# Kernel optimization log

Measured on AMD Instinct MI355X. Metric: run time of the kernel, lower is better.

Reference implementation:

```python
import jax, jax.numpy as jnp
import numpy as np

EMBED_DIM = 1024
NUM_HEADS = 16
HEAD_DIM = EMBED_DIM // NUM_HEADS
FF_DIM = 4096
EPS = 1e-5


def layer_norm(x, gamma, beta):
    mu = jnp.mean(x, axis=-1, keepdims=True)
    var = jnp.var(x, axis=-1, keepdims=True)
    return (x - mu) * jax.lax.rsqrt(var + EPS) * gamma + beta


def setup_inputs() -> dict:
    key = jax.random.key(0)
    ks = jax.random.split(key, 10)
    B, S = 2, 2048
    sd = 1.0 / np.sqrt(EMBED_DIM)
    sf = 1.0 / np.sqrt(FF_DIM)
    return {
        "x": jax.random.normal(ks[0], (B, S, EMBED_DIM), jnp.float32),
        # grouped QKV: 3*num_heads groups, each embed_dim -> head_dim
        "Wqkv": jax.random.normal(ks[1], (3 * NUM_HEADS, EMBED_DIM, HEAD_DIM), jnp.float32) * sd,
        "bqkv": jnp.zeros((3 * NUM_HEADS, HEAD_DIM), jnp.float32),
        "Wo": jax.random.normal(ks[2], (EMBED_DIM, EMBED_DIM), jnp.float32) * sd,
        "bo": jnp.zeros((EMBED_DIM,), jnp.float32),
        "W1": jax.random.normal(ks[3], (EMBED_DIM, FF_DIM), jnp.float32) * sd,
        "b1": jnp.zeros((FF_DIM,), jnp.float32),
        "W2": jax.random.normal(ks[4], (FF_DIM, EMBED_DIM), jnp.float32) * sf,
        "b2": jnp.zeros((EMBED_DIM,), jnp.float32),
        "ln1_g": jnp.ones((EMBED_DIM,), jnp.float32),
        "ln1_b": jnp.zeros((EMBED_DIM,), jnp.float32),
        "ln2_g": jnp.ones((EMBED_DIM,), jnp.float32),
        "ln2_b": jnp.zeros((EMBED_DIM,), jnp.float32),
    }


def reference(x, Wqkv, bqkv, Wo, bo, W1, b1, W2, b2, ln1_g, ln1_b, ln2_g, ln2_b):
    B, S, D = x.shape
    normed = layer_norm(x, ln1_g, ln1_b)
    # grouped QKV projection: group g gets its own (D, head_dim) weight
    qkv = jnp.einsum('bsd,gdh->bgsh', normed, Wqkv) + bqkv[None, :, None, :]
    qkv = qkv.reshape(B, 3, NUM_HEADS, S, HEAD_DIM)
    q, k, v = qkv[:, 0], qkv[:, 1], qkv[:, 2]  # each [B, H, S, hd]
    attn = jnp.einsum('bhqd,bhkd->bhqk', q, k) / np.sqrt(HEAD_DIM)
    attn = jax.nn.softmax(attn, axis=-1)
    out = jnp.einsum('bhqk,bhkd->bhqd', attn, v)
    out = out.transpose(0, 2, 1, 3).reshape(B, S, D)
    out = out @ Wo + bo
    x = x + out
    normed2 = layer_norm(x, ln2_g, ln2_b)
    ff = jax.nn.relu(normed2 @ W1 + b1) @ W2 + b2
    return x + ff
```

## Files before the change

### kernel.cpp

```cpp
#include <hip/hip_runtime.h>
#include <stdint.h>

#define SEQ    2048
#define NB     2
#define NHEADS 16
#define HDIM   64
#define EMBED  1024
#define NROWS  (NB*SEQ)
#define QKVSZ  ((size_t)NB*NHEADS*SEQ*HDIM)

typedef __attribute__((ext_vector_type(8))) short short8;
typedef __attribute__((ext_vector_type(4))) float float4v;
typedef __attribute__((ext_vector_type(16))) float float16v;
typedef __attribute__((ext_vector_type(2))) unsigned int uint2v;
typedef __attribute__((ext_vector_type(4))) unsigned int uint4v;

__device__ __forceinline__ float b2f(unsigned short h) {
    unsigned int u = ((unsigned int)h) << 16;
    union { unsigned int u; float f; } c; c.u = u; return c.f;
}
__device__ __forceinline__ unsigned short f2b(float f) {
    union { float f; unsigned int u; } c; c.f = f;
    unsigned int u = c.u;
    u += 0x7FFFu + ((u >> 16) & 1u);
    return (unsigned short)(u >> 16);
}
__device__ __forceinline__ unsigned int fbits(float f) {
    union { float f; unsigned int u; } c; c.f = f; return c.u;
}
__device__ __forceinline__ unsigned int cvtpk_bf16(float lo, float hi) {
    unsigned int r;
    asm("v_cvt_pk_bf16_f32 %0, %1, %2" : "=v"(r) : "v"(lo), "v"(hi));
    return r;
}

__device__ __forceinline__ void gload_lds16(const void* g, void* l) {
    __builtin_amdgcn_global_load_lds(
        (const __attribute__((address_space(1))) unsigned int*)g,
        (__attribute__((address_space(3))) unsigned int*)l, 16, 0, 0);
}

__device__ __forceinline__ int probe_f32(const void* probe) {
    return ((const unsigned short*)probe)[0] == 0;
}
__device__ __forceinline__ float lde(const void* base, size_t off, int f32) {
    return f32 ? ((const float*)base)[off] : b2f(((const unsigned short*)base)[off]);
}
__device__ __forceinline__ void ste(void* base, size_t off, float v, int f32) {
    if (f32) ((float*)base)[off] = v;
    else     ((unsigned short*)base)[off] = f2b(v);
}

__global__ __launch_bounds__(256) void ln_kernel(
    const void* __restrict__ x,
    const void* __restrict__ g,
    const void* __restrict__ b,
    unsigned short* __restrict__ out,
    const void* __restrict__ probe)
{
    int f32 = probe_f32(probe);
    int row = blockIdx.x;
    int t = threadIdx.x;
    float v0, v1, v2, v3;
    if (f32) {
        float4 rv = ((const float4*)x)[(size_t)row * (EMBED / 4) + t];
        v0 = rv.x; v1 = rv.y; v2 = rv.z; v3 = rv.w;
    } else {
        ushort4 rv = ((const ushort4*)((const unsigned short*)x + (size_t)row * EMBED))[t];
        v0 = b2f(rv.x); v1 = b2f(rv.y); v2 = b2f(rv.z); v3 = b2f(rv.w);
    }
    float s  = v0 + v1 + v2 + v3;
    float sq = v0*v0 + v1*v1 + v2*v2 + v3*v3;
    #pragma unroll
    for (int off = 32; off > 0; off >>= 1) {
        s  += __shfl_xor(s,  off);
        sq += __shfl_xor(sq, off);
    }
    __shared__ float red[8];
    int lane = t & 63, wv = t >> 6;
    if (lane == 0) { red[wv] = s; red[wv + 4] = sq; }
    __syncthreads();
    s  = red[0] + red[1] + red[2] + red[3];
    sq = red[4] + red[5] + red[6] + red[7];
    float mu  = s * (1.0f / EMBED);
    float var = sq * (1.0f / EMBED) - mu * mu;
    float rs  = rsqrtf(var + 1e-5f);
    float g0 = lde(g, t*4+0, f32), g1 = lde(g, t*4+1, f32);
    float g2 = lde(g, t*4+2, f32), g3 = lde(g, t*4+3, f32);
    float b0 = lde(b, t*4+0, f32), b1 = lde(b, t*4+1, f32);
    float b2 = lde(b, t*4+2, f32), b3 = lde(b, t*4+3, f32);
    ushort4 ov;
    ov.x = f2b((v0 - mu) * rs * g0 + b0);
    ov.y = f2b((v1 - mu) * rs * g1 + b1);
    ov.z = f2b((v2 - mu) * rs * g2 + b2);
    ov.w = f2b((v3 - mu) * rs * g3 + b3);
    ((ushort4*)(out + (size_t)row * EMBED))[t] = ov;
}

template<int QKV>
__global__ __launch_bounds__(256) void transpose_kernel(
    const void* __restrict__ in,
    unsigned short* __restrict__ out, int K, int N,
    const void* __restrict__ probe)
{
    __shared__ unsigned short t[64 * 68];
    int f32 = probe_f32(probe);
    int tid = threadIdx.x;
    int n0 = blockIdx.x * 64, k0 = blockIdx.y * 64;
    #pragma unroll
    for (int i = 0; i < 4; i++) {
        int id = tid + i * 256;
        int kr = id >> 4, nc = (id & 15) * 4;
        size_t srcoff;
        if (QKV) srcoff = ((size_t)(n0 >> 6) << 16) + (size_t)(k0 + kr) * 64 + nc;
        else     srcoff = (size_t)(k0 + kr) * N + n0 + nc;
        ushort4 val;
        if (f32) {
            float4 rv = *(const float4*)((const float*)in + srcoff);
            val.x = f2b(rv.x); val.y = f2b(rv.y); val.z = f2b(rv.z); val.w = f2b(rv.w);
        } else {
            val = *(const ushort4*)((const unsigned short*)in + srcoff);
        }
        *(ushort4*)&t[kr * 68 + nc] = val;
    }
    __syncthreads();
    #pragma unroll
    for (int i = 0; i < 4; i++) {
        int id = tid + i * 256;
        int nr = id >> 4, kc = (id & 15) * 4;
        ushort4 o;
        o.x = t[(kc + 0) * 68 + nr];
        o.y = t[(kc + 1) * 68 + nr];
        o.z = t[(kc + 2) * 68 + nr];
        o.w = t[(kc + 3) * 68 + nr];
        *(ushort4*)(out + (size_t)(n0 + nr) * K + k0 + kc) = o;
    }
}

template<int DO_RELU, int HAS_BIAS, int OUTMODE>
__global__ __launch_bounds__(512) void gemm256_kernel(
    const unsigned short* __restrict__ A,
    const unsigned short* __restrict__ Bt,
    const void* __restrict__ bias,
    void* __restrict__ out,
    int M, int N, int Kloc, int ldA, int ldB,
    const void* __restrict__ probe)
{
    __shared__ unsigned short Als[2][256 * 64];
    __shared__ unsigned short Bls[2][256 * 64];
    int f32 = probe_f32(probe);
    int tid = threadIdx.x;
    int lane = tid & 63, wv = tid >> 6;
    int lq = lane >> 4, lr = lane & 15;
    int wr = wv >> 2, wc = wv & 3;
    int m0 = blockIdx.y * 256, n0 = blockIdx.x * 256;
    int k0 = blockIdx.z * Kloc;

    int srow = tid >> 3;
    int sch  = (tid & 7) ^ (srow & 7);
    const unsigned short* ga = A  + (size_t)(m0 + srow) * ldA + k0 + sch * 8;
    const unsigned short* gb = Bt + (size_t)(n0 + srow) * ldB + k0 + sch * 8;
    int ldst = tid * 8;
    int rx = lr & 7;

    float4v acc[8][4];
    #pragma unroll
    for (int i = 0; i < 8; i++)
        #pragma unroll
        for (int j = 0; j < 4; j++)
            { acc[i][j][0] = 0.f; acc[i][j][1] = 0.f; acc[i][j][2] = 0.f; acc[i][j][3] = 0.f; }

    int nkt = Kloc >> 6;
    #pragma unroll
    for (int u = 0; u < 4; u++)
        gload_lds16(ga + (size_t)u * 64 * ldA, &Als[0][u * 4096 + ldst]);
    #pragma unroll
    for (int u = 0; u < 4; u++)
        gload_lds16(gb + (size_t)u * 64 * ldB, &Bls[0][u * 4096 + ldst]);

    for (int kt = 0; kt < nkt; kt++) {
        int cur = kt & 1, nxt = cur ^ 1;
        if (kt + 1 < nkt) {
            int ko = (kt + 1) * 64;
            #pragma unroll
            for (int u = 0; u < 4; u++)
                gload_lds16(ga + (size_t)u * 64 * ldA + ko, &Als[nxt][u * 4096 + ldst]);
            asm volatile("s_waitcnt vmcnt(4)" ::: "memory");
        } else {
            asm volatile("s_waitcnt vmcnt(0)" ::: "memory");
        }
        __builtin_amdgcn_s_barrier();
        asm volatile("" ::: "memory");
        {
            short8 af[8], bf[4];
            #pragma unroll
            for (int mt = 0; mt < 8; mt++)
                af[mt] = *(const short8*)(
                    &Als[cur][(wr * 128 + mt * 16 + lr) * 64 + ((lq ^ rx) * 8)]);
            #pragma unroll
            for (int nt = 0; nt < 4; nt++)
                bf[nt] = *(const short8*)(
                    &Bls[cur][(wc * 64 + nt * 16 + lr) * 64 + ((lq ^ rx) * 8)]);
            __builtin_amdgcn_s_setprio(1);
            #pragma unroll
            for (int mt = 0; mt < 8; mt++)
                #pragma unroll
                for (int nt = 0; nt < 4; nt++)
                    acc[mt][nt] = __builtin_amdgcn_mfma_f32_16x16x32_bf16(af[mt], bf[nt], acc[mt][nt], 0, 0, 0);
            __builtin_amdgcn_s_setprio(0);
        }
        if (kt + 1 < nkt) {
            int ko = (kt + 1) * 64;
            #pragma unroll
            for (int u = 0; u < 4; u++)
                gload_lds16(gb + (size_t)u * 64 * ldB + ko, &Bls[nxt][u * 4096 + ldst]);
        }
        {
            short8 af[8], bf[4];
            #pragma unroll
            for (int mt = 0; mt < 8; mt++)
                af[mt] = *(const short8*)(
                    &Als[cur][(wr * 128 + mt * 16 + lr) * 64 + (((4 + lq) ^ rx) * 8)]);
            #pragma unroll
            for (int nt = 0; nt < 4; nt++)
                bf[nt] = *(const short8*)(
                    &Bls[cur][(wc * 64 + nt * 16 + lr) * 64 + (((4 + lq) ^ rx) * 8)]);
            __builtin_amdgcn_s_setprio(1);
            #pragma unroll
            for (int mt = 0; mt < 8; mt++)
                #pragma unroll
                for (int nt = 0; nt < 4; nt++)
                    acc[mt][nt] = __builtin_amdgcn_mfma_f32_16x16x32_bf16(af[mt], bf[nt], acc[mt][nt], 0, 0, 0);
            __builtin_amdgcn_s_setprio(0);
        }
        asm volatile("s_waitcnt lgkmcnt(0)" ::: "memory");
        __builtin_amdgcn_s_barrier();
    }

    if (OUTMODE == 3) {
        float* po = (float*)out + (size_t)blockIdx.z * M * N;
        #pragma unroll
        for (int mt = 0; mt < 8; mt++)
            #pragma unroll
            for (int nt = 0; nt < 4; nt++)
                #pragma unroll
                for (int rg = 0; rg < 4; rg++) {
                    int rr = m0 + wr * 128 + mt * 16 + lq * 4 + rg;
                    int cc = n0 + wc * 64 + nt * 16 + lr;
                    po[(size_t)rr * N + cc] = acc[mt][nt][rg];
                }
    } else if (OUTMODE == 2) {
        #pragma unroll
        for (int mt = 0; mt < 8; mt++) {
            int rrb = m0 + wr * 128 + mt * 16 + lq * 4;
            int bb = rrb >> 11, ss = rrb & 2047;
            #pragma unroll
            for (int nt = 0; nt < 4; nt++) {
                int cc = n0 + wc * 64 + nt * 16 + lr;
                int gg = cc >> 6, hd = cc & 63;
                int ty = gg >> 4, hh = gg & 15;
                float vv[4];
                #pragma unroll
                for (int rg = 0; rg < 4; rg++) {
                    float v = acc[mt][nt][rg];
                    if (HAS_BIAS) v += lde(bias, (size_t)cc, f32);
                    vv[rg] = v;
                }
                if (ty < 2) {
                    unsigned short* p = (unsigned short*)out + (size_t)ty * QKVSZ +
                        (((size_t)(bb * NHEADS + hh) * SEQ + ss) * HDIM) + hd;
                    #pragma unroll
                    for (int rg = 0; rg < 4; rg++) p[(size_t)rg * HDIM] = f2b(vv[rg]);
                } else {
                    ushort4 pk;
                    pk.x = f2b(vv[0]); pk.y = f2b(vv[1]);
                    pk.z = f2b(vv[2]); pk.w = f2b(vv[3]);
                    *(ushort4*)((unsigned short*)out + 2 * QKVSZ +
                        ((size_t)(bb * NHEADS + hh) * HDIM + hd) * SEQ + ss) = pk;
                }
            }
        }
    } else {
        #pragma unroll
        for (int mt = 0; mt < 8; mt++)
            #pragma unroll
            for (int nt = 0; nt < 4; nt++)
                #pragma unroll
                for (int rg = 0; rg < 4; rg++) {
                    int rr = m0 + wr * 128 + mt * 16 + lq * 4 + rg;
                    int cc = n0 + wc * 64 + nt * 16 + lr;
                    float v = acc[mt][nt][rg];
                    if (HAS_BIAS) v += lde(bias, (size_t)cc, f32);
                    if (DO_RELU) v = v > 0.f ? v : 0.f;
                    ((unsigned short*)out)[(size_t)rr * N + cc] = f2b(v);
                }
    }
}

__global__ __launch_bounds__(256) void ff2_combine_kernel(
    const float* __restrict__ part,
    const void* __restrict__ b2,
    void* __restrict__ xout,
    const void* __restrict__ probe)
{
    int f32 = probe_f32(probe);
    int row = blockIdx.x;
    int t = threadIdx.x;
    const size_t MN = (size_t)NROWS * EMBED;
    size_t base = (size_t)row * EMBED + t * 4;
    float4 p0 = *(const float4*)(part + base);
    float4 p1 = *(const float4*)(part + MN + base);
    float4 p2 = *(const float4*)(part + 2 * MN + base);
    float4 p3 = *(const float4*)(part + 3 * MN + base);
    float s0 = (p0.x + p1.x) + (p2.x + p3.x);
    float s1 = (p0.y + p1.y) + (p2.y + p3.y);
    float s2 = (p0.z + p1.z) + (p2.z + p3.z);
    float s3 = (p0.w + p1.w) + (p2.w + p3.w);
    int c = t * 4;
    s0 += lde(b2, c + 0, f32) + lde(xout, base + 0, f32);
    s1 += lde(b2, c + 1, f32) + lde(xout, base + 1, f32);
    s2 += lde(b2, c + 2, f32) + lde(xout, base + 2, f32);
    s3 += lde(b2, c + 3, f32) + lde(xout, base + 3, f32);
    ste(xout, base + 0, s0, f32);
    ste(xout, base + 1, s1, f32);
    ste(xout, base + 2, s2, f32);
    ste(xout, base + 3, s3, f32);
}

template<int DO_RELU, int HAS_BIAS, int HAS_RES, int OUTMODE>
__global__ __launch_bounds__(256) void gemm64_kernel(
    const unsigned short* __restrict__ A,
    const unsigned short* __restrict__ Bt,
    const void* __restrict__ bias,
    const void* __restrict__ res,
    void* __restrict__ out,
    int M, int N, int K, int ldA, int ldB,
    const void* __restrict__ probe)
{
    __shared__ unsigned short Als[2][64 * 32];
    __shared__ unsigned short Bls[2][64 * 32];
    int f32 = probe_f32(probe);
    int tid = threadIdx.x;
    int lane = tid & 63, wv = tid >> 6;
    int lq = lane >> 4, lr = lane & 15;
    int moff = (wv >> 1) * 32, noff = (wv & 1) * 32;
    int m0 = blockIdx.y * 64, n0 = blockIdx.x * 64;

    int rA = tid >> 2, jA = tid & 3;
    int jjA = jA ^ ((rA >> 1) & 3);
    const unsigned short* ga = A  + (size_t)(m0 + rA) * ldA + jjA * 8;
    const unsigned short* gb = Bt + (size_t)(n0 + rA) * ldB + jjA * 8;

    int fch = (lq ^ ((lr >> 1) & 3)) * 8;

    float4v acc[2][2];
    #pragma unroll
    for (int i = 0; i < 2; i++)
        #pragma unroll
        for (int j = 0; j < 2; j++)
            { acc[i][j][0] = 0.f; acc[i][j][1] = 0.f; acc[i][j][2] = 0.f; acc[i][j][3] = 0.f; }

    gload_lds16(ga, &Als[0][(size_t)tid * 8]);
    gload_lds16(gb, &Bls[0][(size_t)tid * 8]);

    int nkt = K >> 5;
    for (int kt = 0; kt < nkt; kt++) {
        int cur = kt & 1, nxt = cur ^ 1;
        __syncthreads();
        if (kt + 1 < nkt) {
            int ko = (kt + 1) * 32;
            gload_lds16(ga + ko, &Als[nxt][(size_t)tid * 8]);
            gload_lds16(gb + ko, &Bls[nxt][(size_t)tid * 8]);
        }
        short8 af[2], bfr[2];
        #pragma unroll
        for (int mt = 0; mt < 2; mt++)
            af[mt] = *(const short8*)(&Als[cur][(moff + mt * 16 + lr) * 32 + fch]);
        #pragma unroll
        for (int nt = 0; nt < 2; nt++)
            bfr[nt] = *(const short8*)(&Bls[cur][(noff + nt * 16 + lr) * 32 + fch]);
        #pragma unroll
        for (int mt = 0; mt < 2; mt++)
            #pragma unroll
            for (int nt = 0; nt < 2; nt++)
                acc[mt][nt] = __builtin_amdgcn_mfma_f32_16x16x32_bf16(af[mt], bfr[nt], acc[mt][nt], 0, 0, 0);
    }

    #pragma unroll
    for (int mt = 0; mt < 2; mt++) {
        #pragma unroll
        for (int nt = 0; nt < 2; nt++) {
            #pragma unroll
            for (int rg = 0; rg < 4; rg++) {
                int rr = m0 + moff + mt * 16 + lq * 4 + rg;
                int cc = n0 + noff + nt * 16 + lr;
                float v = acc[mt][nt][rg];
                if (HAS_BIAS) v += lde(bias, (size_t)cc, f32);
                if (DO_RELU) v = v > 0.f ? v : 0.f;
                if (HAS_RES) v += lde(res, (size_t)rr * N + cc, f32);
                if (OUTMODE == 1) ste(out, (size_t)rr * N + cc, v, f32);
                else ((unsigned short*)out)[(size_t)rr * N + cc] = f2b(v);
            }
        }
    }
}

__global__ __launch_bounds__(256) void attn_kernel(
    const unsigned short* __restrict__ qb,
    const unsigned short* __restrict__ kb,
    const unsigned short* __restrict__ vtb,
    unsigned short* __restrict__ outb)
{
    __shared__ unsigned short Kls[2][64 * 64];
    __shared__ unsigned short Vls[2][64 * 64];
    int tid = threadIdx.x;
    int lane = tid & 63, wv = tid >> 6;
    int l31 = lane & 31, hh = lane >> 5;
    int bh = blockIdx.y;
    int b = bh >> 4, head = bh & 15;
    const unsigned short* q  = qb  + (size_t)bh * SEQ * HDIM;
    const unsigned short* k  = kb  + (size_t)bh * SEQ * HDIM;
    const unsigned short* vt = vtb + (size_t)bh * HDIM * SEQ;
    int q0w = blockIdx.x * 128 + wv * 32;

    const float C2 = 0.18033688011112042f;

    short8 qf[4];
    #pragma unroll
    for (int c = 0; c < 4; c++) {
        short8 raw = *(const short8*)(q + (size_t)(q0w + l31) * HDIM + c * 16 + hh * 8);
        #pragma unroll
        for (int j = 0; j < 8; j++)
            qf[c][j] = (short)f2b(b2f((unsigned short)raw[j]) * C2);
    }

    int rS = tid >> 3;
    int jjS = (tid & 7) ^ (rS & 7);
    const unsigned short* gk0 = k + (size_t)rS * HDIM + jjS * 8;
    const unsigned short* gk1 = k + (size_t)(rS + 32) * HDIM + jjS * 8;
    const unsigned short* gv0 = vt + (size_t)rS * SEQ + jjS * 8;
    const unsigned short* gv1 = vt + (size_t)(rS + 32) * SEQ + jjS * 8;

    float l_part = 0.f;
    float16v o0, o1;
    #pragma unroll
    for (int i = 0; i < 16; i++) { o0[i] = 0.f; o1[i] = 0.f; }

    gload_lds16(gk0, &Kls[0][(size_t)tid * 8]);
    gload_lds16(gk1, &Kls[0][(size_t)(tid + 256) * 8]);
    gload_lds16(gv0, &Vls[0][(size_t)tid * 8]);
    gload_lds16(gv1, &Vls[0][(size_t)(tid + 256) * 8]);

    for (int kt = 0; kt < SEQ / 64; kt++) {
        int cur = kt & 1, nxt = cur ^ 1;
        __syncthreads();
        if (kt + 1 < SEQ / 64) {
            int k0n = (kt + 1) * 64;
            gload_lds16(gk0 + (size_t)k0n * HDIM, &Kls[nxt][(size_t)tid * 8]);
            gload_lds16(gk1 + (size_t)k0n * HDIM, &Kls[nxt][(size_t)(tid + 256) * 8]);
            gload_lds16(gv0 + k0n, &Vls[nxt][(size_t)tid * 8]);
            gload_lds16(gv1 + k0n, &Vls[nxt][(size_t)(tid + 256) * 8]);
        }

        #pragma unroll
        for (int kb2 = 0; kb2 < 2; kb2++) {
            float16v st;
            #pragma unroll
            for (int i = 0; i < 16; i++) st[i] = 0.f;
            int r = kb2 * 32 + l31;
            int rx = r & 7;
            #pragma unroll
            for (int c = 0; c < 4; c++) {
                short8 kf = *(const short8*)(
                    &Kls[cur][r * 64 + (((2 * c + hh) ^ rx) * 8)]);
                st = __builtin_amdgcn_mfma_f32_32x32x16_bf16(kf, qf[c], st, 0, 0, 0);
            }
            float p[16];
            #pragma unroll
            for (int rg = 0; rg < 16; rg++) {
                p[rg] = __builtin_amdgcn_exp2f(st[rg]);
                l_part += p[rg];
            }
            int rv0 = l31, rv1 = 32 + l31;
            int rxv = l31 & 7;
            #pragma unroll
            for (int s = 0; s < 2; s++) {
                unsigned int a1 = cvtpk_bf16(p[8*s+0], p[8*s+1]);
                unsigned int a2 = cvtpk_bf16(p[8*s+2], p[8*s+3]);
                unsigned int b1 = cvtpk_bf16(p[8*s+4], p[8*s+5]);
                unsigned int b2 = cvtpk_bf16(p[8*s+6], p[8*s+7]);
                uint2v r1 = __builtin_amdgcn_permlane32_swap(a1, b1, false, false);
                uint2v r2 = __builtin_amdgcn_permlane32_swap(a2, b2, false, false);
                union { uint4v u; short8 s8; } pun;
                pun.u.x = r1.x; pun.u.y = r2.x; pun.u.z = r1.y; pun.u.w = r2.y;
                short8 pf = pun.s8;
                int g = kb2 * 2 + s;
                short8 vf0 = *(const short8*)(
                    &Vls[cur][rv0 * 64 + (((2 * g + hh) ^ rxv) * 8)]);
                o0 = __builtin_amdgcn_mfma_f32_32x32x16_bf16(pf, vf0, o0, 0, 0, 0);
                short8 vf1 = *(const short8*)(
                    &Vls[cur][rv1 * 64 + (((2 * g + hh) ^ rxv) * 8)]);
                o1 = __builtin_amdgcn_mfma_f32_32x32x16_bf16(pf, vf1, o1, 0, 0, 0);
            }
        }
    }

    l_part += __shfl_xor(l_part, 32);
    float linv_me = 1.f / l_part;
    #pragma unroll
    for (int rg = 0; rg < 16; rg++) {
        int qrow = (rg & 3) + 8 * (rg >> 2) + 4 * hh;
        float linv = __shfl(linv_me, qrow);
        size_t rowbase = ((size_t)(b * SEQ + q0w + qrow)) * EMBED + head * HDIM;
        outb[rowbase + l31]      = f2b(o0[rg] * linv);
        outb[rowbase + 32 + l31] = f2b(o1[rg] * linv);
    }
}

extern "C" void kernel_launch(void* const* d_in, const int* in_sizes, int n_in,
                              void* d_out, int out_size, void* d_ws, size_t ws_size,
                              hipStream_t stream)
{
    (void)in_sizes; (void)n_in; (void)out_size;
    const void* x    = d_in[0];
    const void* Wqkv = d_in[1];
    const void* bqkv = d_in[2];
    const void* Wo   = d_in[3];
    const void* bo   = d_in[4];
    const void* W1   = d_in[5];
    const void* b1   = d_in[6];
    const void* W2   = d_in[7];
    const void* b2   = d_in[8];
    const void* g1   = d_in[9];
    const void* be1  = d_in[10];
    const void* g2   = d_in[11];
    const void* be2  = d_in[12];
    const void* probe = g1;

    char* ws = (char*)d_ws;
    const size_t MB = 1024 * 1024;
    unsigned short* tmp1  = (unsigned short*)(ws + 0 * MB);
    unsigned short* qkv   = (unsigned short*)(ws + 8 * MB);
    unsigned short* WoT   = (unsigned short*)(ws + 8 * MB);
    unsigned short* W1T   = (unsigned short*)(ws + 8 * MB);
    unsigned short* W2T   = (unsigned short*)(ws + 8 * MB);
    unsigned short* h1    = (unsigned short*)(ws + 16 * MB);
    float*          part  = (float*)(ws + 48 * MB);
    unsigned short* WqkvT = (unsigned short*)d_out;
    bool splitk_ok = ws_size >= (size_t)112 * MB;

    transpose_kernel<1><<<dim3(3072 / 64, 1024 / 64), 256, 0, stream>>>(Wqkv, WqkvT, 1024, 3072, probe);
    ln_kernel<<<dim3(NROWS), 256, 0, stream>>>(x, g1, be1, tmp1, probe);
    gemm256_kernel<0, 1, 2><<<dim3(3072 / 256, NROWS / 256), 512, 0, stream>>>(
        tmp1, WqkvT, bqkv, qkv, NROWS, 3072, 1024, 1024, 1024, probe);
    attn_kernel<<<dim3(SEQ / 128, NB * NHEADS), 256, 0, stream>>>(
        qkv, qkv + QKVSZ, qkv + 2 * QKVSZ, tmp1);
    transpose_kernel<0><<<dim3(1024 / 64, 1024 / 64), 256, 0, stream>>>(Wo, WoT, 1024, 1024, probe);
    gemm64_kernel<0, 1, 1, 1><<<dim3(1024 / 64, NROWS / 64), 256, 0, stream>>>(
        tmp1, WoT, bo, x, d_out, NROWS, 1024, 1024, 1024, 1024, probe);
    ln_kernel<<<dim3(NROWS), 256, 0, stream>>>(d_out, g2, be2, tmp1, probe);
    transpose_kernel<0><<<dim3(4096 / 64, 1024 / 64), 256, 0, stream>>>(W1, W1T, 1024, 4096, probe);
    gemm256_kernel<1, 1, 0><<<dim3(4096 / 256, NROWS / 256), 512, 0, stream>>>(
        tmp1, W1T, b1, h1, NROWS, 4096, 1024, 1024, 1024, probe);
    transpose_kernel<0><<<dim3(1024 / 64, 4096 / 64), 256, 0, stream>>>(W2, W2T, 4096, 1024, probe);
    if (splitk_ok) {
        gemm256_kernel<0, 0, 3><<<dim3(1024 / 256, NROWS / 256, 4), 512, 0, stream>>>(
            h1, W2T, nullptr, part, NROWS, 1024, 1024, 4096, 4096, probe);
        ff2_combine_kernel<<<dim3(NROWS), 256, 0, stream>>>(part, b2, d_out, probe);
    } else {
        gemm64_kernel<0, 1, 1, 1><<<dim3(1024 / 64, NROWS / 64), 256, 0, stream>>>(
            h1, W2T, b2, d_out, d_out, NROWS, 1024, 4096, 4096, 4096, probe);
    }
}
```

Baseline: 390.4 us.

## Split 256x256 GEMM tile into four 128x128 quadrant phases with staged prefetch

Restructures the 256x256 bf16 GEMM main loop into four quadrant phases, each computing a 128x128 sub-tile of the output. A and B are loaded into LDS as 128-row halves, and the prefetch of the next K-tile is interleaved across the phases with finer-grained vmcnt waits and barriers. The goal is to overlap global-to-LDS loads with MFMA work more evenly and to reuse A/B fragments held in registers across adjacent quadrants. The cost is four times as many barriers per K-step and a more fragile schedule that depends on wait counts.

```diff
diff --git a/kernel.cpp b/kernel.cpp
--- a/kernel.cpp
+++ b/kernel.cpp
@@ -146,8 +146,8 @@
     int M, int N, int Kloc, int ldA, int ldB,
     const void* __restrict__ probe)
 {
-    __shared__ unsigned short Als[2][256 * 64];
-    __shared__ unsigned short Bls[2][256 * 64];
+    __shared__ unsigned short Als[2][2][128 * 64];
+    __shared__ unsigned short Bls[2][2][128 * 64];
     int f32 = probe_f32(probe);
     int tid = threadIdx.x;
     int lane = tid & 63, wv = tid >> 6;
@@ -163,138 +163,166 @@
     int ldst = tid * 8;
     int rx = lr & 7;
 
-    float4v acc[8][4];
-    #pragma unroll
-    for (int i = 0; i < 8; i++)
-        #pragma unroll
-        for (int j = 0; j < 4; j++)
-            { acc[i][j][0] = 0.f; acc[i][j][1] = 0.f; acc[i][j][2] = 0.f; acc[i][j][3] = 0.f; }
+    auto stageA = [&](int d, int h, int ko) {
+        gload_lds16(ga + (size_t)(h * 128) * ldA + ko, &Als[d][h][ldst]);
+        gload_lds16(ga + (size_t)(h * 128 + 64) * ldA + ko, &Als[d][h][4096 + ldst]);
+    };
+    auto stageB = [&](int d, int h, int ko) {
+        gload_lds16(gb + (size_t)(h * 128) * ldB + ko, &Bls[d][h][ldst]);
+        gload_lds16(gb + (size_t)(h * 128 + 64) * ldB + ko, &Bls[d][h][4096 + ldst]);
+    };
+    auto rdA = [&](int cur_, int qr, short8 (&af)[4][2]) {
+        #pragma unroll
+        for (int mt = 0; mt < 4; mt++)
+            #pragma unroll
+            for (int c = 0; c < 2; c++)
+                af[mt][c] = *(const short8*)(&Als[cur_][qr][
+                    (wr * 64 + mt * 16 + lr) * 64 + (((c * 4 + lq) ^ rx) * 8)]);
+    };
+    auto rdB = [&](int cur_, int qc, short8 (&bf)[2][2]) {
+        #pragma unroll
+        for (int nt = 0; nt < 2; nt++)
+            #pragma unroll
+            for (int c = 0; c < 2; c++)
+                bf[nt][c] = *(const short8*)(&Bls[cur_][qc][
+                    (wc * 32 + nt * 16 + lr) * 64 + (((c * 4 + lq) ^ rx) * 8)]);
+    };
+    auto FMA = [&](short8 (&af)[4][2], short8 (&bf)[2][2], float4v (&aq)[4][2]) {
+        __builtin_amdgcn_s_setprio(1);
+        #pragma unroll
+        for (int c = 0; c < 2; c++)
+            #pragma unroll
+            for (int mt = 0; mt < 4; mt++)
+                #pragma unroll
+                for (int nt = 0; nt < 2; nt++)
+                    aq[mt][nt] = __builtin_amdgcn_mfma_f32_16x16x32_bf16(
+                        af[mt][c], bf[nt][c], aq[mt][nt], 0, 0, 0);
+        __builtin_amdgcn_s_setprio(0);
+    };
+
+    float4v acc00[4][2], acc01[4][2], acc11[4][2], acc10[4][2];
+    #pragma unroll
+    for (int i = 0; i < 4; i++)
+        #pragma unroll
+        for (int j = 0; j < 2; j++) {
+            acc00[i][j] = float4v{0.f, 0.f, 0.f, 0.f};
+            acc01[i][j] = float4v{0.f, 0.f, 0.f, 0.f};
+            acc11[i][j] = float4v{0.f, 0.f, 0.f, 0.f};
+            acc10[i][j] = float4v{0.f, 0.f, 0.f, 0.f};
+        }
 
     int nkt = Kloc >> 6;
-    #pragma unroll
-    for (int u = 0; u < 4; u++)
-        gload_lds16(ga + (size_t)u * 64 * ldA, &Als[0][u * 4096 + ldst]);
-    #pragma unroll
-    for (int u = 0; u < 4; u++)
-        gload_lds16(gb + (size_t)u * 64 * ldB, &Bls[0][u * 4096 + ldst]);
+    stageA(0, 0, 0); stageB(0, 0, 0); stageB(0, 1, 0); stageA(0, 1, 0);
 
     for (int kt = 0; kt < nkt; kt++) {
         int cur = kt & 1, nxt = cur ^ 1;
-        if (kt + 1 < nkt) {
-            int ko = (kt + 1) * 64;
-            #pragma unroll
-            for (int u = 0; u < 4; u++)
-                gload_lds16(ga + (size_t)u * 64 * ldA + ko, &Als[nxt][u * 4096 + ldst]);
-            asm volatile("s_waitcnt vmcnt(4)" ::: "memory");
-        } else {
-            asm volatile("s_waitcnt vmcnt(0)" ::: "memory");
-        }
-        __builtin_amdgcn_s_barrier();
-        asm volatile("" ::: "memory");
-        {
-            short8 af[8], bf[4];
-            #pragma unroll
-            for (int mt = 0; mt < 8; mt++)
-                af[mt] = *(const short8*)(
-                    &Als[cur][(wr * 128 + mt * 16 + lr) * 64 + ((lq ^ rx) * 8)]);
-            #pragma unroll
-            for (int nt = 0; nt < 4; nt++)
-                bf[nt] = *(const short8*)(
-                    &Bls[cur][(wc * 64 + nt * 16 + lr) * 64 + ((lq ^ rx) * 8)]);
-            __builtin_amdgcn_s_setprio(1);
-            #pragma unroll
-            for (int mt = 0; mt < 8; mt++)
+        bool pf = (kt + 1 < nkt);
+        int ko = (kt + 1) * 64;
+        short8 af[4][2], bf[2][2];
+
+        if (pf) { stageA(nxt, 0, ko);
+                  asm volatile("s_waitcnt vmcnt(6)" ::: "memory"); }
+        else      asm volatile("s_waitcnt vmcnt(0)" ::: "memory");
+        __builtin_amdgcn_s_barrier();
+        asm volatile("" ::: "memory");
+        rdA(cur, 0, af); rdB(cur, 0, bf);
+        FMA(af, bf, acc00);
+        asm volatile("" ::: "memory");
+        __builtin_amdgcn_s_barrier();
+
+        if (pf) { stageB(nxt, 0, ko);
+                  asm volatile("s_waitcnt vmcnt(6)" ::: "memory"); }
+        else      asm volatile("s_waitcnt vmcnt(0)" ::: "memory");
+        __builtin_amdgcn_s_barrier();
+        asm volatile("" ::: "memory");
+        rdB(cur, 1, bf);
+        FMA(af, bf, acc01);
+        asm volatile("" ::: "memory");
+        __builtin_amdgcn_s_barrier();
+
+        if (pf) { stageB(nxt, 1, ko);
+                  asm volatile("s_waitcnt vmcnt(6)" ::: "memory"); }
+        else      asm volatile("s_waitcnt vmcnt(0)" ::: "memory");
+        __builtin_amdgcn_s_barrier();
+        asm volatile("" ::: "memory");
+        rdA(cur, 1, af);
+        FMA(af, bf, acc11);
+        asm volatile("" ::: "memory");
+        __builtin_amdgcn_s_barrier();
+
+        if (pf) { stageA(nxt, 1, ko);
+                  asm volatile("s_waitcnt vmcnt(6)" ::: "memory"); }
+        else      asm volatile("s_waitcnt vmcnt(0)" ::: "memory");
+        __builtin_amdgcn_s_barrier();
+        asm volatile("" ::: "memory");
+        rdB(cur, 0, bf);
+        FMA(af, bf, acc10);
+        asm volatile("" ::: "memory");
+        __builtin_amdgcn_s_barrier();
+    }
+
+    auto storeQ = [&](int qr, int qc, float4v (&aq)[4][2]) {
+        if (OUTMODE == 3) {
+            float* po = (float*)out + (size_t)blockIdx.z * M * N;
+            #pragma unroll
+            for (int mt = 0; mt < 4; mt++)
                 #pragma unroll
-                for (int nt = 0; nt < 4; nt++)
-                    acc[mt][nt] = __builtin_amdgcn_mfma_f32_16x16x32_bf16(af[mt], bf[nt], acc[mt][nt], 0, 0, 0);
-            __builtin_amdgcn_s_setprio(0);
-        }
-        if (kt + 1 < nkt) {
-            int ko = (kt + 1) * 64;
-            #pragma unroll
-            for (int u = 0; u < 4; u++)
-                gload_lds16(gb + (size_t)u * 64 * ldB + ko, &Bls[nxt][u * 4096 + ldst]);
-        }
-        {
-            short8 af[8], bf[4];
-            #pragma unroll
-            for (int mt = 0; mt < 8; mt++)
-                af[mt] = *(const short8*)(
-                    &Als[cur][(wr * 128 + mt * 16 + lr) * 64 + (((4 + lq) ^ rx) * 8)]);
-            #pragma unroll
-            for (int nt = 0; nt < 4; nt++)
-                bf[nt] = *(const short8*)(
-                    &Bls[cur][(wc * 64 + nt * 16 + lr) * 64 + (((4 + lq) ^ rx) * 8)]);
-            __builtin_amdgcn_s_setprio(1);
-            #pragma unroll
-            for (int mt = 0; mt < 8; mt++)
+                for (int nt = 0; nt < 2; nt++)
+                    #pragma unroll
+                    for (int rg = 0; rg < 4; rg++) {
+                        int rr = m0 + qr * 128 + wr * 64 + mt * 16 + lq * 4 + rg;
+                        int cc = n0 + qc * 128 + wc * 32 + nt * 16 + lr;
+                        po[(size_t)rr * N + cc] = aq[mt][nt][rg];
+                    }
+        } else if (OUTMODE == 2) {
+            #pragma unroll
+            for (int mt = 0; mt < 4; mt++) {
+                int rrb = m0 + qr * 128 + wr * 64 + mt * 16 + lq * 4;
+                int bb = rrb >> 11, ss = rrb & 2047;
                 #pragma unroll
-                for (int nt = 0; nt < 4; nt++)
-                    acc[mt][nt] = __builtin_amdgcn_mfma_f32_16x16x32_bf16(af[mt], bf[nt], acc[mt][nt], 0, 0, 0);
-            __builtin_amdgcn_s_setprio(0);
-        }
-        asm volatile("s_waitcnt lgkmcnt(0)" ::: "memory");
-        __builtin_amdgcn_s_barrier();
-    }
-
-    if (OUTMODE == 3) {
-        float* po = (float*)out + (size_t)blockIdx.z * M * N;
-        #pragma unroll
-        for (int mt = 0; mt < 8; mt++)
-            #pragma unroll
-            for (int nt = 0; nt < 4; nt++)
-                #pragma unroll
-                for (int rg = 0; rg < 4; rg++) {
-                    int rr = m0 + wr * 128 + mt * 16 + lq * 4 + rg;
-                    int cc = n0 + wc * 64 + nt * 16 + lr;
-                    po[(size_t)rr * N + cc] = acc[mt][nt][rg];
-                }
-    } else if (OUTMODE == 2) {
-        #pragma unroll
-        for (int mt = 0; mt < 8; mt++) {
-            int rrb = m0 + wr * 128 + mt * 16 + lq * 4;
-            int bb = rrb >> 11, ss = rrb & 2047;
-            #pragma unroll
-            for (int nt = 0; nt < 4; nt++) {
-                int cc = n0 + wc * 64 + nt * 16 + lr;
-                int gg = cc >> 6, hd = cc & 63;
-                int ty = gg >> 4, hh = gg & 15;
-                float vv[4];
-                #pragma unroll
-                for (int rg = 0; rg < 4; rg++) {
-                    float v = acc[mt][nt][rg];
-                    if (HAS_BIAS) v += lde(bias, (size_t)cc, f32);
-                    vv[rg] = v;
-                }
-                if (ty < 2) {
-                    unsigned short* p = (unsigned short*)out + (size_t)ty * QKVSZ +
-                        (((size_t)(bb * NHEADS + hh) * SEQ + ss) * HDIM) + hd;
+                for (int nt = 0; nt < 2; nt++) {
+                    int cc = n0 + qc * 128 + wc * 32 + nt * 16 + lr;
+                    int gg = cc >> 6, hd = cc & 63;
+                    int ty = gg >> 4, hh = gg & 15;
+                    float vv[4];
                     #pragma unroll
-                    for (int rg = 0; rg < 4; rg++) p[(size_t)rg * HDIM] = f2b(vv[rg]);
-                } else {
-                    ushort4 pk;
-                    pk.x = f2b(vv[0]); pk.y = f2b(vv[1]);
-                    pk.z = f2b(vv[2]); pk.w = f2b(vv[3]);
-                    *(ushort4*)((unsigned short*)out + 2 * QKVSZ +
-                        ((size_t)(bb * NHEADS + hh) * HDIM + hd) * SEQ + ss) = pk;
+                    for (int rg = 0; rg < 4; rg++) {
+                        float v = aq[mt][nt][rg];
+                        if (HAS_BIAS) v += lde(bias, (size_t)cc, f32);
+                        vv[rg] = v;
+                    }
+                    if (ty < 2) {
+                        unsigned short* p = (unsigned short*)out + (size_t)ty * QKVSZ +
+                            (((size_t)(bb * NHEADS + hh) * SEQ + ss) * HDIM) + hd;
+                        #pragma unroll
+                        for (int rg = 0; rg < 4; rg++) p[(size_t)rg * HDIM] = f2b(vv[rg]);
+                    } else {
+                        ushort4 pk;
+                        pk.x = f2b(vv[0]); pk.y = f2b(vv[1]);
+                        pk.z = f2b(vv[2]); pk.w = f2b(vv[3]);
+                        *(ushort4*)((unsigned short*)out + 2 * QKVSZ +
+                            ((size_t)(bb * NHEADS + hh) * HDIM + hd) * SEQ + ss) = pk;
+                    }
                 }
             }
+        } else {
+            #pragma unroll
+            for (int mt = 0; mt < 4; mt++)
+                #pragma unroll
+                for (int nt = 0; nt < 2; nt++)
+                    #pragma unroll
+                    for (int rg = 0; rg < 4; rg++) {
+                        int rr = m0 + qr * 128 + wr * 64 + mt * 16 + lq * 4 + rg;
+                        int cc = n0 + qc * 128 + wc * 32 + nt * 16 + lr;
+                        float v = aq[mt][nt][rg];
+                        if (HAS_BIAS) v += lde(bias, (size_t)cc, f32);
+                        if (DO_RELU) v = v > 0.f ? v : 0.f;
+                        ((unsigned short*)out)[(size_t)rr * N + cc] = f2b(v);
+                    }
         }
-    } else {
-        #pragma unroll
-        for (int mt = 0; mt < 8; mt++)
-            #pragma unroll
-            for (int nt = 0; nt < 4; nt++)
-                #pragma unroll
-                for (int rg = 0; rg < 4; rg++) {
-                    int rr = m0 + wr * 128 + mt * 16 + lq * 4 + rg;
-                    int cc = n0 + wc * 64 + nt * 16 + lr;
-                    float v = acc[mt][nt][rg];
-                    if (HAS_BIAS) v += lde(bias, (size_t)cc, f32);
-                    if (DO_RELU) v = v > 0.f ? v : 0.f;
-                    ((unsigned short*)out)[(size_t)rr * N + cc] = f2b(v);
-                }
-    }
+    };
+    storeQ(0, 0, acc00); storeQ(0, 1, acc01);
+    storeQ(1, 1, acc11); storeQ(1, 0, acc10);
 }
 
 __global__ __launch_bounds__(256) void ff2_combine_kernel(
```

After: 419.9 us. 1.08x slower.

## Add 8-phase quadrant-pipelined 256x256 GEMM for the FF1 projection

Applied to the files above, without the earlier changes.

Adds a new 256x256-tile GEMM kernel that splits each K-tile into four 128x128 quadrants, double-buffers them in LDS, and interleaves MFMA work on one quadrant with async global-to-LDS loads and fragment reads for the next, using fine-grained vmcnt waits, barriers and s_setprio. Only the FF1 (W1, ReLU) GEMM is switched to it. The goal is to hide load and barrier latency behind matrix-core work. It adds many barriers per K-tile and more complex scheduling, and relies on Kloc being a multiple of 128.

```diff
diff --git a/kernel.cpp b/kernel.cpp
--- a/kernel.cpp
+++ b/kernel.cpp
@@ -295,6 +295,150 @@
                     ((unsigned short*)out)[(size_t)rr * N + cc] = f2b(v);
                 }
     }
+}
+
+template<int DO_RELU, int HAS_BIAS, int OUTMODE>
+__global__ __launch_bounds__(512) void gemm256p8_kernel(
+    const unsigned short* __restrict__ A,
+    const unsigned short* __restrict__ Bt,
+    const void* __restrict__ bias,
+    void* __restrict__ out,
+    int M, int N, int Kloc, int ldA, int ldB,
+    const void* __restrict__ probe)
+{
+    __shared__ unsigned short Als[2][2][128 * 64];
+    __shared__ unsigned short Bls[2][2][128 * 64];
+    int f32 = probe_f32(probe);
+    int tid = threadIdx.x;
+    int lane = tid & 63, wv = tid >> 6;
+    int lq = lane >> 4, lr = lane & 15;
+    int wr = wv >> 2, wc = wv & 3;
+    int m0 = blockIdx.y * 256, n0 = blockIdx.x * 256;
+    int k0 = blockIdx.z * Kloc;
+
+    int srow = tid >> 3;
+    int sch  = (tid & 7) ^ (srow & 7);
+    const unsigned short* ga = A  + (size_t)(m0 + srow) * ldA + k0 + sch * 8;
+    const unsigned short* gb = Bt + (size_t)(n0 + srow) * ldB + k0 + sch * 8;
+    int ldst = tid * 8;
+    int rx = lr & 7;
+
+    auto stA = [&](int d, int h, int ko) {
+        gload_lds16(ga + (size_t)(h * 128) * ldA + ko, &Als[d][h][ldst]);
+        gload_lds16(ga + (size_t)(h * 128 + 64) * ldA + ko, &Als[d][h][4096 + ldst]);
+    };
+    auto stB = [&](int d, int h, int ko) {
+        gload_lds16(gb + (size_t)(h * 128) * ldB + ko, &Bls[d][h][ldst]);
+        gload_lds16(gb + (size_t)(h * 128 + 64) * ldB + ko, &Bls[d][h][4096 + ldst]);
+    };
+    auto rdA = [&](int d, int qm, short8 (&af)[4][2]) {
+        #pragma unroll
+        for (int mt = 0; mt < 4; mt++)
+            #pragma unroll
+            for (int c = 0; c < 2; c++)
+                af[mt][c] = *(const short8*)(&Als[d][qm][
+                    (wr * 64 + mt * 16 + lr) * 64 + (((c * 4 + lq) ^ rx) * 8)]);
+    };
+    auto rdB = [&](int d, int qn, short8 (&bf)[2][2]) {
+        #pragma unroll
+        for (int nt = 0; nt < 2; nt++)
+            #pragma unroll
+            for (int c = 0; c < 2; c++)
+                bf[nt][c] = *(const short8*)(&Bls[d][qn][
+                    (wc * 32 + nt * 16 + lr) * 64 + (((c * 4 + lq) ^ rx) * 8)]);
+    };
+    auto MM = [&](short8 (&af)[4][2], short8 (&bf)[2][2], float4v (&aq)[4][2]) {
+        __builtin_amdgcn_s_setprio(1);
+        #pragma unroll
+        for (int c = 0; c < 2; c++)
+            #pragma unroll
+            for (int mt = 0; mt < 4; mt++)
+                #pragma unroll
+                for (int nt = 0; nt < 2; nt++)
+                    aq[mt][nt] = __builtin_amdgcn_mfma_f32_16x16x32_bf16(
+                        af[mt][c], bf[nt][c], aq[mt][nt], 0, 0, 0);
+        __builtin_amdgcn_s_setprio(0);
+    };
+    #define VMC(n)  asm volatile("s_waitcnt vmcnt(" #n ")" ::: "memory")
+    #define BARF()  do { __builtin_amdgcn_s_barrier(); \
+                         asm volatile("" ::: "memory"); } while (0)
+
+    float4v acc00[4][2], acc01[4][2], acc11[4][2], acc10[4][2];
+    #pragma unroll
+    for (int i = 0; i < 4; i++)
+        #pragma unroll
+        for (int j = 0; j < 2; j++) {
+            acc00[i][j] = float4v{0.f, 0.f, 0.f, 0.f};
+            acc01[i][j] = float4v{0.f, 0.f, 0.f, 0.f};
+            acc11[i][j] = float4v{0.f, 0.f, 0.f, 0.f};
+            acc10[i][j] = float4v{0.f, 0.f, 0.f, 0.f};
+        }
+    short8 af0[4][2], af1[4][2], bf0[2][2], bf1[2][2];
+
+    int nkt = Kloc >> 6;
+    int npair = nkt >> 1;
+
+    stA(0, 0, 0); stB(0, 0, 0); stB(0, 1, 0); stA(0, 1, 0);
+    VMC(4); BARF();
+    rdA(0, 0, af0); rdB(0, 0, bf0);
+
+    for (int p = 0; p < npair - 1; p++) {
+        int koB  = (2 * p + 1) * 64;
+        int koA2 = (2 * p + 2) * 64;
+        MM(af0, bf0, acc00); stA(1, 0, koB); VMC(4); BARF(); rdB(0, 1, bf1);
+        MM(af0, bf1, acc01); stB(1, 0, koB); VMC(4); BARF(); rdA(0, 1, af1);
+        MM(af1, bf1, acc11); stB(1, 1, koB);         BARF(); rdB(0, 0, bf0);
+        MM(af1, bf0, acc10); stA(1, 1, koB); VMC(4); BARF(); rdA(1, 0, af0); rdB(1, 0, bf1);
+        MM(af0, bf1, acc00); stA(0, 0, koA2); VMC(4); BARF(); rdB(1, 1, bf0);
+        MM(af0, bf0, acc01); stB(0, 0, koA2); VMC(4); BARF(); rdA(1, 1, af1);
+        MM(af1, bf0, acc11); stB(0, 1, koA2);         BARF(); rdB(1, 0, bf1);
+        MM(af1, bf1, acc10); stA(0, 1, koA2); VMC(4); BARF(); rdA(0, 0, af0); rdB(0, 0, bf0);
+    }
+    {
+        int koB = (nkt - 1) * 64;
+        MM(af0, bf0, acc00); stA(1, 0, koB); VMC(4); BARF(); rdB(0, 1, bf1);
+        MM(af0, bf1, acc01); stB(1, 0, koB); VMC(4); BARF(); rdA(0, 1, af1);
+        MM(af1, bf1, acc11); stB(1, 1, koB);         BARF(); rdB(0, 0, bf0);
+        MM(af1, bf0, acc10); stA(1, 1, koB); VMC(4); BARF(); rdA(1, 0, af0); rdB(1, 0, bf1);
+        MM(af0, bf1, acc00);                  VMC(2); BARF(); rdB(1, 1, bf0);
+        MM(af0, bf0, acc01);                  VMC(0); BARF(); rdA(1, 1, af1);
+        MM(af1, bf0, acc11);                          BARF(); rdB(1, 0, bf1);
+        MM(af1, bf1, acc10);
+    }
+    #undef VMC
+    #undef BARF
+
+    auto storeQ = [&](int qr, int qc, float4v (&aq)[4][2]) {
+        if (OUTMODE == 3) {
+            float* po = (float*)out + (size_t)blockIdx.z * M * N;
+            #pragma unroll
+            for (int mt = 0; mt < 4; mt++)
+                #pragma unroll
+                for (int nt = 0; nt < 2; nt++)
+                    #pragma unroll
+                    for (int rg = 0; rg < 4; rg++) {
+                        int rr = m0 + qr * 128 + wr * 64 + mt * 16 + lq * 4 + rg;
+                        int cc = n0 + qc * 128 + wc * 32 + nt * 16 + lr;
+                        po[(size_t)rr * N + cc] = aq[mt][nt][rg];
+                    }
+        } else {
+            #pragma unroll
+            for (int mt = 0; mt < 4; mt++)
+                #pragma unroll
+                for (int nt = 0; nt < 2; nt++)
+                    #pragma unroll
+                    for (int rg = 0; rg < 4; rg++) {
+                        int rr = m0 + qr * 128 + wr * 64 + mt * 16 + lq * 4 + rg;
+                        int cc = n0 + qc * 128 + wc * 32 + nt * 16 + lr;
+                        float v = aq[mt][nt][rg];
+                        if (HAS_BIAS) v += lde(bias, (size_t)cc, f32);
+                        if (DO_RELU) v = v > 0.f ? v : 0.f;
+                        ((unsigned short*)out)[(size_t)rr * N + cc] = f2b(v);
+                    }
+        }
+    };
+    storeQ(0, 0, acc00); storeQ(0, 1, acc01);
+    storeQ(1, 1, acc11); storeQ(1, 0, acc10);
 }
 
 __global__ __launch_bounds__(256) void ff2_combine_kernel(
@@ -560,7 +704,7 @@
         tmp1, WoT, bo, x, d_out, NROWS, 1024, 1024, 1024, 1024, probe);
     ln_kernel<<<dim3(NROWS), 256, 0, stream>>>(d_out, g2, be2, tmp1, probe);
     transpose_kernel<0><<<dim3(4096 / 64, 1024 / 64), 256, 0, stream>>>(W1, W1T, 1024, 4096, probe);
-    gemm256_kernel<1, 1, 0><<<dim3(4096 / 256, NROWS / 256), 512, 0, stream>>>(
+    gemm256p8_kernel<1, 1, 0><<<dim3(4096 / 256, NROWS / 256), 512, 0, stream>>>(
         tmp1, W1T, b1, h1, NROWS, 4096, 1024, 1024, 1024, probe);
     transpose_kernel<0><<<dim3(1024 / 64, 4096 / 64), 256, 0, stream>>>(W2, W2T, 4096, 1024, probe);
     if (splitk_ok) {
```

Measured after the change: 388.7 us. No clear change (-0.4%).
